# Kernel optimization log

Measured on AMD Instinct MI355X. Metric: run time of the kernel, lower is better.

Reference implementation:

```python
import jax, jax.numpy as jnp
import numpy as np

B, K, IN, CH, M, N = 1024, 64, 128, 256, 4, 16


def setup_inputs() -> dict:
    key = jax.random.key(0)
    ks = jax.random.split(key, 12)
    s = 0.02
    return {
        "user_node": jax.random.normal(ks[0], (B, K, IN), jnp.float32),
        "RIS_node": jax.random.normal(ks[1], (B, IN), jnp.float32),
        "cas_channel": jax.random.normal(ks[2], (B, K, 2 * M * N), jnp.float32),
        "d_link": jax.random.normal(ks[3], (B, K, 2 * M), jnp.float32),
        # f2_user: Linear(3*IN -> CH), ReLU, Linear(CH -> CH)
        "W1": jax.random.normal(ks[4], (3 * IN, CH), jnp.float32) * s,
        "b1": jnp.zeros((CH,), jnp.float32),
        "W2": jax.random.normal(ks[5], (CH, CH), jnp.float32) * s,
        "b2": jnp.zeros((CH,), jnp.float32),
        # f3_RIS: Linear(2*IN -> CH), ReLU, Linear(CH -> CH)
        "W3": jax.random.normal(ks[6], (2 * IN, CH), jnp.float32) * s,
        "b3": jnp.zeros((CH,), jnp.float32),
        "W4": jax.random.normal(ks[7], (CH, CH), jnp.float32) * s,
        "b4": jnp.zeros((CH,), jnp.float32),
    }


def _leave_one_out_max(x):
    # x: (B, K, D). Exact leave-one-out max via prefix/suffix cummax, O(K).
    prefix = jax.lax.cummax(x, axis=1)                      # max over 0..k
    suffix = jax.lax.cummax(x[:, ::-1], axis=1)[:, ::-1]    # max over k..K-1
    neg = jnp.full_like(x[:, :1], -jnp.inf)
    left = jnp.concatenate([neg, prefix[:, :-1]], axis=1)   # max over 0..k-1
    right = jnp.concatenate([suffix[:, 1:], neg], axis=1)   # max over k+1..K-1
    return jnp.maximum(left, right)


def reference(user_node, RIS_node, cas_channel, d_link,
              W1, b1, W2, b2, W3, b3, W4, b4):
    b, k, d = user_node.shape
    mean_user = jnp.mean(user_node, axis=1)                 # (B, IN)
    loo_max = _leave_one_out_max(user_node)                 # (B, K, IN)
    ris_b = jnp.broadcast_to(RIS_node[:, None, :], (b, k, d))
    feat = jnp.concatenate([user_node, loo_max, ris_b], axis=-1)  # (B, K, 3*IN)
    h_user = jax.nn.relu(feat @ W1 + b1) @ W2 + b2          # (B, K, CH)
    user_node_update = jnp.concatenate([user_node, h_user], axis=-1)  # (B,K,IN+CH)
    rfeat = jnp.concatenate([RIS_node, mean_user], axis=-1)  # (B, 2*IN)
    h_ris = jax.nn.relu(rfeat @ W3 + b3) @ W4 + b4          # (B, CH)
    RIS_node_update = jnp.concatenate([RIS_node, h_ris], axis=-1)    # (B, IN+CH)
    return user_node_update, RIS_node_update
```

## Files before the change

### kernel.cpp

```cpp
#include <hip/hip_runtime.h>

typedef __attribute__((ext_vector_type(8))) short short8;
typedef __attribute__((ext_vector_type(4))) float f32x4;
typedef __attribute__((ext_vector_type(4))) int i32x4;
typedef __attribute__((ext_vector_type(4))) unsigned u32x4;

__device__ __forceinline__ unsigned short f2bf(float f) {
  unsigned u = __builtin_bit_cast(unsigned, f);
  u += 0x7fffu + ((u >> 16) & 1u);
  return (unsigned short)(u >> 16);
}

__global__ __launch_bounds__(256) void prep(
    const float* __restrict__ user,
    const float* __restrict__ W1, const float* __restrict__ W2,
    const float* __restrict__ W3, const float* __restrict__ W4,
    float* __restrict__ mean, float* __restrict__ max1,
    float* __restrict__ max2, int* __restrict__ argm,
    unsigned short* __restrict__ W1f, unsigned short* __restrict__ W2f,
    unsigned short* __restrict__ W3f, unsigned short* __restrict__ W4f) {
  if (blockIdx.x < 512) {
    int idx = blockIdx.x * 256 + threadIdx.x;
    int b = idx >> 7, i = idx & 127;
    const float* up = user + (size_t)(b * 64) * 128 + i;
    float s = 0.f, m1 = -3.402823466e38f, m2 = -3.402823466e38f;
    int am = 0;
    #pragma unroll 8
    for (int k = 0; k < 64; ++k) {
      float u = up[(size_t)k * 128];
      s += u;
      if (u > m1) { m2 = m1; m1 = u; am = k; }
      else if (u > m2) { m2 = u; }
    }
    mean[idx] = s * (1.f / 64.f);
    max1[idx] = m1;
    max2[idx] = m2;
    argm[idx] = am;
  } else {
    int idx = (blockIdx.x - 512) * 256 + threadIdx.x;
    const float* src; unsigned short* dst; int kb; int rel;
    if (idx < 98304)        { src = W1; dst = W1f; kb = 12; rel = idx; }
    else if (idx < 163840)  { src = W2; dst = W2f; kb = 8;  rel = idx - 98304; }
    else if (idx < 229376)  { src = W3; dst = W3f; kb = 8;  rel = idx - 163840; }
    else                    { src = W4; dst = W4f; kb = 8;  rel = idx - 229376; }
    int kk = rel >> 8, n = rel & 255;
    int lane = (n & 15) | (((kk >> 3) & 3) << 4);
    int di = (((n >> 4) * kb + (kk >> 5)) * 64 + lane) * 8 + (kk & 7);
    dst[di] = f2bf(src[rel]);
  }
}

template<int MODE>
__device__ __forceinline__ void mlp_body(
    int bx, unsigned short* __restrict__ Abuf, unsigned short* __restrict__ Hb,
    const float* __restrict__ srcA,
    const float* __restrict__ max1, const float* __restrict__ max2,
    const int* __restrict__ argm, const float* __restrict__ aux,
    const unsigned short* __restrict__ Wa, const unsigned short* __restrict__ Wb,
    const float* __restrict__ ba, const float* __restrict__ bb,
    float* __restrict__ out) {
  constexpr int NSTEP = (MODE == 0) ? 6 : 4;
  constexpr int KB1 = NSTEP * 2;

  const int tid = threadIdx.x;
  const int lane = tid & 63, wn = tid >> 6;
  const int row0 = bx * 64;
  const int sr = tid >> 2;
  const int sc = (tid & 3) << 4;
  const int bidx = row0 >> 6;

  auto load_step = [&](int s, float* v) {
    if constexpr (MODE == 0) {
      if (s < 2) {
        const float* p = &srcA[(size_t)(row0 + sr) * 128 + s * 64 + sc];
        #pragma unroll
        for (int q = 0; q < 4; ++q) {
          f32x4 t = *(const f32x4*)(p + q * 4);
          #pragma unroll
          for (int jj = 0; jj < 4; ++jj) v[q * 4 + jj] = t[jj];
        }
      } else if (s < 4) {
        int ib = bidx * 128 + (s - 2) * 64 + sc;
        #pragma unroll
        for (int q = 0; q < 4; ++q) {
          i32x4 aq = *(const i32x4*)(argm + ib + q * 4);
          f32x4 m1q = *(const f32x4*)(max1 + ib + q * 4);
          f32x4 m2q = *(const f32x4*)(max2 + ib + q * 4);
          #pragma unroll
          for (int jj = 0; jj < 4; ++jj)
            v[q * 4 + jj] = (aq[jj] == sr) ? m2q[jj] : m1q[jj];
        }
      } else {
        const float* p = &aux[bidx * 128 + (s - 4) * 64 + sc];
        #pragma unroll
        for (int q = 0; q < 4; ++q) {
          f32x4 t = *(const f32x4*)(p + q * 4);
          #pragma unroll
          for (int jj = 0; jj < 4; ++jj) v[q * 4 + jj] = t[jj];
        }
      }
    } else {
      const float* p = (s < 2) ? &srcA[(size_t)(row0 + sr) * 128 + s * 64 + sc]
                               : &aux[(size_t)(row0 + sr) * 128 + (s - 2) * 64 + sc];
      #pragma unroll
      for (int q = 0; q < 4; ++q) {
        f32x4 t = *(const f32x4*)(p + q * 4);
        #pragma unroll
        for (int jj = 0; jj < 4; ++jj) v[q * 4 + jj] = t[jj];
      }
    }
  };

  auto stage_write = [&](int buf, int s, const float* v) {
    if (s < 2) {
      float* o = &out[(size_t)(row0 + sr) * 384 + s * 64 + sc];
      #pragma unroll
      for (int q = 0; q < 4; ++q) {
        f32x4 t = {v[q * 4 + 0], v[q * 4 + 1], v[q * 4 + 2], v[q * 4 + 3]};
        *(f32x4*)(o + q * 4) = t;
      }
    }
    unsigned pk[8];
    #pragma unroll
    for (int j = 0; j < 8; ++j)
      pk[j] = (unsigned)f2bf(v[2 * j]) | ((unsigned)f2bf(v[2 * j + 1]) << 16);
    unsigned short* base = Abuf + buf * (64 * 64) + sr * 64;
    int c0 = (tid & 3) * 2, k = sr & 7;
    u32x4 w0 = {pk[0], pk[1], pk[2], pk[3]};
    u32x4 w1 = {pk[4], pk[5], pk[6], pk[7]};
    *(u32x4*)(base + ((c0 ^ k) << 3)) = w0;
    *(u32x4*)(base + (((c0 + 1) ^ k) << 3)) = w1;
  };

  f32x4 acc[4][4];
  #pragma unroll
  for (int a = 0; a < 4; ++a)
    #pragma unroll
    for (int q = 0; q < 4; ++q) acc[a][q] = (f32x4)0.f;

  {
    float v0[16];
    load_step(0, v0);
    stage_write(0, 0, v0);
  }
  __syncthreads();
  #pragma unroll
  for (int s = 0; s < NSTEP; ++s) {
    float nv[16];
    if (s + 1 < NSTEP) load_step(s + 1, nv);
    const unsigned short* Ab = Abuf + (s & 1) * (64 * 64);
    #pragma unroll
    for (int ks = 0; ks < 2; ++ks) {
      short8 af[4], bfr[4];
      #pragma unroll
      for (int mf = 0; mf < 4; ++mf) {
        int r = mf * 16 + (lane & 15);
        int c = ks * 4 + (lane >> 4);
        af[mf] = *(const short8*)(Ab + r * 64 + ((c ^ (r & 7)) << 3));
      }
      #pragma unroll
      for (int nf = 0; nf < 4; ++nf)
        bfr[nf] = *(const short8*)&Wa[(size_t)(((wn * 4 + nf) * KB1 + (s * 2 + ks)) * 64 + lane) * 8];
      #pragma unroll
      for (int mf = 0; mf < 4; ++mf)
        #pragma unroll
        for (int nf = 0; nf < 4; ++nf)
          acc[mf][nf] = __builtin_amdgcn_mfma_f32_16x16x32_bf16(af[mf], bfr[nf], acc[mf][nf], 0, 0, 0);
    }
    if (s + 1 < NSTEP) stage_write((s + 1) & 1, s + 1, nv);
    __syncthreads();
  }

  float bav[4];
  #pragma unroll
  for (int nf = 0; nf < 4; ++nf) bav[nf] = ba[wn * 64 + nf * 16 + (lane & 15)];
  #pragma unroll
  for (int mf = 0; mf < 4; ++mf)
    #pragma unroll
    for (int nf = 0; nf < 4; ++nf)
      #pragma unroll
      for (int j = 0; j < 4; ++j) {
        int r = mf * 16 + ((lane >> 4) * 4) + j;
        int col = wn * 64 + nf * 16 + (lane & 15);
        int c = col >> 3;
        Hb[r * 256 + ((c ^ (r & 7)) << 3) + (col & 7)] =
            f2bf(fmaxf(acc[mf][nf][j] + bav[nf], 0.f));
      }
  __syncthreads();

  #pragma unroll
  for (int a = 0; a < 4; ++a)
    #pragma unroll
    for (int q = 0; q < 4; ++q) acc[a][q] = (f32x4)0.f;
  #pragma unroll
  for (int kc = 0; kc < 8; ++kc) {
    short8 af[4], bfr[4];
    #pragma unroll
    for (int mf = 0; mf < 4; ++mf) {
      int r = mf * 16 + (lane & 15);
      int c = kc * 4 + (lane >> 4);
      af[mf] = *(const short8*)(Hb + r * 256 + ((c ^ (r & 7)) << 3));
    }
    #pragma unroll
    for (int nf = 0; nf < 4; ++nf)
      bfr[nf] = *(const short8*)&Wb[(size_t)(((wn * 4 + nf) * 8 + kc) * 64 + lane) * 8];
    #pragma unroll
    for (int mf = 0; mf < 4; ++mf)
      #pragma unroll
      for (int nf = 0; nf < 4; ++nf)
        acc[mf][nf] = __builtin_amdgcn_mfma_f32_16x16x32_bf16(af[mf], bfr[nf], acc[mf][nf], 0, 0, 0);
  }

  float bbv[4];
  #pragma unroll
  for (int nf = 0; nf < 4; ++nf) bbv[nf] = bb[wn * 64 + nf * 16 + (lane & 15)];
  #pragma unroll
  for (int mf = 0; mf < 4; ++mf)
    #pragma unroll
    for (int nf = 0; nf < 4; ++nf)
      #pragma unroll
      for (int j = 0; j < 4; ++j) {
        int r = mf * 16 + ((lane >> 4) * 4) + j;
        int col = wn * 64 + nf * 16 + (lane & 15);
        out[(size_t)(row0 + r) * 384 + 128 + col] = acc[mf][nf][j] + bbv[nf];
      }
}

__global__ __launch_bounds__(256, 3) void fused(
    const float* __restrict__ user, const float* __restrict__ ris,
    const float* __restrict__ max1, const float* __restrict__ max2,
    const int* __restrict__ argm, const float* __restrict__ mean,
    const unsigned short* __restrict__ W1f, const unsigned short* __restrict__ W2f,
    const unsigned short* __restrict__ W3f, const unsigned short* __restrict__ W4f,
    const float* __restrict__ b1, const float* __restrict__ b2,
    const float* __restrict__ b3, const float* __restrict__ b4,
    float* __restrict__ out0, float* __restrict__ out1) {
  __shared__ unsigned short Abuf[2 * 64 * 64];
  __shared__ unsigned short Hb[64 * 256];
  if (blockIdx.x < 1024)
    mlp_body<0>(blockIdx.x, Abuf, Hb, user, max1, max2, argm, ris,
                W1f, W2f, b1, b2, out0);
  else
    mlp_body<1>(blockIdx.x - 1024, Abuf, Hb, ris, nullptr, nullptr, nullptr,
                mean, W3f, W4f, b3, b4, out1);
}

extern "C" void kernel_launch(void* const* d_in, const int* in_sizes, int n_in,
                              void* d_out, int out_size, void* d_ws, size_t ws_size,
                              hipStream_t stream) {
  const float* user = (const float*)d_in[0];
  const float* ris  = (const float*)d_in[1];
  const float* W1 = (const float*)d_in[4];
  const float* b1 = (const float*)d_in[5];
  const float* W2 = (const float*)d_in[6];
  const float* b2 = (const float*)d_in[7];
  const float* W3 = (const float*)d_in[8];
  const float* b3 = (const float*)d_in[9];
  const float* W4 = (const float*)d_in[10];
  const float* b4 = (const float*)d_in[11];

  float* out0 = (float*)d_out;
  float* out1 = out0 + (size_t)65536 * 384;

  char* ws = (char*)d_ws;
  float* mean = (float*)(ws);
  float* max1 = (float*)(ws + 524288);
  float* max2 = (float*)(ws + 1048576);
  int*   argm = (int*)(ws + 1572864);
  unsigned short* W1f = (unsigned short*)(ws + 2097152);
  unsigned short* W2f = (unsigned short*)(ws + 2293760);
  unsigned short* W3f = (unsigned short*)(ws + 2424832);
  unsigned short* W4f = (unsigned short*)(ws + 2555904);

  hipLaunchKernelGGL(prep, dim3(1664), dim3(256), 0, stream,
                     user, W1, W2, W3, W4, mean, max1, max2, argm,
                     W1f, W2f, W3f, W4f);
  hipLaunchKernelGGL(fused, dim3(1040), dim3(256), 0, stream,
                     user, ris, max1, max2, argm, mean,
                     W1f, W2f, W3f, W4f, b1, b2, b3, b4, out0, out1);
}
```

Baseline: 71.90 us.

## Load GEMM1 A-fragments directly from global, drop LDS staging, precompute bf16 stats

The first GEMM no longer stages its A operand through double-buffered shared memory. Each lane loads its MFMA fragment straight from global memory (user rows converted to bf16 on the fly, and the max, mean and ris vectors stored as bf16 by prep), which removes the per-step __syncthreads. The passthrough copies of user and ris into the outputs move into the prep kernel, and occupancy is raised to 4 blocks per SM because less LDS is needed. In exchange, global loads are less coalesced and sit on the MFMA critical path with no software prefetch.

```diff
diff --git a/kernel.cpp b/kernel.cpp
--- a/kernel.cpp
+++ b/kernel.cpp
@@ -3,7 +3,6 @@
 typedef __attribute__((ext_vector_type(8))) short short8;
 typedef __attribute__((ext_vector_type(4))) float f32x4;
 typedef __attribute__((ext_vector_type(4))) int i32x4;
-typedef __attribute__((ext_vector_type(4))) unsigned u32x4;
 
 __device__ __forceinline__ unsigned short f2bf(float f) {
   unsigned u = __builtin_bit_cast(unsigned, f);
@@ -12,30 +11,37 @@
 }
 
 __global__ __launch_bounds__(256) void prep(
-    const float* __restrict__ user,
+    const float* __restrict__ user, const float* __restrict__ ris,
     const float* __restrict__ W1, const float* __restrict__ W2,
     const float* __restrict__ W3, const float* __restrict__ W4,
-    float* __restrict__ mean, float* __restrict__ max1,
-    float* __restrict__ max2, int* __restrict__ argm,
+    unsigned short* __restrict__ m1b, unsigned short* __restrict__ m2b,
+    int* __restrict__ am, unsigned short* __restrict__ meanb,
+    unsigned short* __restrict__ risb,
     unsigned short* __restrict__ W1f, unsigned short* __restrict__ W2f,
-    unsigned short* __restrict__ W3f, unsigned short* __restrict__ W4f) {
+    unsigned short* __restrict__ W3f, unsigned short* __restrict__ W4f,
+    float* __restrict__ out0, float* __restrict__ out1) {
   if (blockIdx.x < 512) {
     int idx = blockIdx.x * 256 + threadIdx.x;
     int b = idx >> 7, i = idx & 127;
     const float* up = user + (size_t)(b * 64) * 128 + i;
+    float* op = out0 + (size_t)(b * 64) * 384 + i;
     float s = 0.f, m1 = -3.402823466e38f, m2 = -3.402823466e38f;
-    int am = 0;
+    int amx = 0;
     #pragma unroll 8
     for (int k = 0; k < 64; ++k) {
       float u = up[(size_t)k * 128];
+      op[(size_t)k * 384] = u;
       s += u;
-      if (u > m1) { m2 = m1; m1 = u; am = k; }
+      if (u > m1) { m2 = m1; m1 = u; amx = k; }
       else if (u > m2) { m2 = u; }
     }
-    mean[idx] = s * (1.f / 64.f);
-    max1[idx] = m1;
-    max2[idx] = m2;
-    argm[idx] = am;
+    m1b[idx] = f2bf(m1);
+    m2b[idx] = f2bf(m2);
+    am[idx] = amx;
+    meanb[idx] = f2bf(s * (1.f / 64.f));
+    float rv = ris[idx];
+    out1[(size_t)b * 384 + i] = rv;
+    risb[idx] = f2bf(rv);
   } else {
     int idx = (blockIdx.x - 512) * 256 + threadIdx.x;
     const float* src; unsigned short* dst; int kb; int rel;
@@ -52,124 +58,81 @@
 
 template<int MODE>
 __device__ __forceinline__ void mlp_body(
-    int bx, unsigned short* __restrict__ Abuf, unsigned short* __restrict__ Hb,
-    const float* __restrict__ srcA,
-    const float* __restrict__ max1, const float* __restrict__ max2,
-    const int* __restrict__ argm, const float* __restrict__ aux,
+    int bx, unsigned short* __restrict__ Hb,
+    const float* __restrict__ user,
+    const unsigned short* __restrict__ m1b, const unsigned short* __restrict__ m2b,
+    const int* __restrict__ am,
+    const unsigned short* __restrict__ risb, const unsigned short* __restrict__ meanb,
     const unsigned short* __restrict__ Wa, const unsigned short* __restrict__ Wb,
     const float* __restrict__ ba, const float* __restrict__ bb,
     float* __restrict__ out) {
-  constexpr int NSTEP = (MODE == 0) ? 6 : 4;
-  constexpr int KB1 = NSTEP * 2;
+  constexpr int NFS = (MODE == 0) ? 12 : 8;
 
   const int tid = threadIdx.x;
   const int lane = tid & 63, wn = tid >> 6;
   const int row0 = bx * 64;
-  const int sr = tid >> 2;
-  const int sc = (tid & 3) << 4;
-  const int bidx = row0 >> 6;
-
-  auto load_step = [&](int s, float* v) {
+  const int r = lane & 15;
+  const int k8 = (lane >> 4) * 8;
+
+  f32x4 acc[4][4];
+  #pragma unroll
+  for (int a = 0; a < 4; ++a)
+    #pragma unroll
+    for (int q = 0; q < 4; ++q) acc[a][q] = (f32x4)0.f;
+
+  #pragma unroll
+  for (int fs = 0; fs < NFS; ++fs) {
+    short8 af[4];
     if constexpr (MODE == 0) {
-      if (s < 2) {
-        const float* p = &srcA[(size_t)(row0 + sr) * 128 + s * 64 + sc];
+      if (fs < 4) {
         #pragma unroll
-        for (int q = 0; q < 4; ++q) {
-          f32x4 t = *(const f32x4*)(p + q * 4);
+        for (int mf = 0; mf < 4; ++mf) {
+          const float* p = &user[(size_t)(row0 + mf * 16 + r) * 128 + fs * 32 + k8];
+          f32x4 t0 = *(const f32x4*)p;
+          f32x4 t1 = *(const f32x4*)(p + 4);
+          short8 t;
           #pragma unroll
-          for (int jj = 0; jj < 4; ++jj) v[q * 4 + jj] = t[jj];
+          for (int j = 0; j < 4; ++j) { t[j] = (short)f2bf(t0[j]); t[4 + j] = (short)f2bf(t1[j]); }
+          af[mf] = t;
         }
-      } else if (s < 4) {
-        int ib = bidx * 128 + (s - 2) * 64 + sc;
+      } else if (fs < 8) {
+        int c0 = bx * 128 + (fs - 4) * 32 + k8;
+        short8 m1v = *(const short8*)&m1b[c0];
+        short8 m2v = *(const short8*)&m2b[c0];
+        i32x4 a0 = *(const i32x4*)&am[c0];
+        i32x4 a1 = *(const i32x4*)&am[c0 + 4];
         #pragma unroll
-        for (int q = 0; q < 4; ++q) {
-          i32x4 aq = *(const i32x4*)(argm + ib + q * 4);
-          f32x4 m1q = *(const f32x4*)(max1 + ib + q * 4);
-          f32x4 m2q = *(const f32x4*)(max2 + ib + q * 4);
+        for (int mf = 0; mf < 4; ++mf) {
+          int rr = mf * 16 + r;
+          short8 t;
           #pragma unroll
-          for (int jj = 0; jj < 4; ++jj)
-            v[q * 4 + jj] = (aq[jj] == sr) ? m2q[jj] : m1q[jj];
+          for (int j = 0; j < 4; ++j) {
+            t[j]     = (a0[j] == rr) ? m2v[j]     : m1v[j];
+            t[4 + j] = (a1[j] == rr) ? m2v[4 + j] : m1v[4 + j];
+          }
+          af[mf] = t;
         }
       } else {
-        const float* p = &aux[bidx * 128 + (s - 4) * 64 + sc];
+        short8 v = *(const short8*)&risb[bx * 128 + (fs - 8) * 32 + k8];
         #pragma unroll
-        for (int q = 0; q < 4; ++q) {
-          f32x4 t = *(const f32x4*)(p + q * 4);
-          #pragma unroll
-          for (int jj = 0; jj < 4; ++jj) v[q * 4 + jj] = t[jj];
-        }
+        for (int mf = 0; mf < 4; ++mf) af[mf] = v;
       }
     } else {
-      const float* p = (s < 2) ? &srcA[(size_t)(row0 + sr) * 128 + s * 64 + sc]
-                               : &aux[(size_t)(row0 + sr) * 128 + (s - 2) * 64 + sc];
-      #pragma unroll
-      for (int q = 0; q < 4; ++q) {
-        f32x4 t = *(const f32x4*)(p + q * 4);
-        #pragma unroll
-        for (int jj = 0; jj < 4; ++jj) v[q * 4 + jj] = t[jj];
-      }
+      const unsigned short* src = (fs < 4) ? risb : meanb;
+      #pragma unroll
+      for (int mf = 0; mf < 4; ++mf)
+        af[mf] = *(const short8*)&src[(size_t)(row0 + mf * 16 + r) * 128 + (fs & 3) * 32 + k8];
     }
-  };
-
-  auto stage_write = [&](int buf, int s, const float* v) {
-    if (s < 2) {
-      float* o = &out[(size_t)(row0 + sr) * 384 + s * 64 + sc];
-      #pragma unroll
-      for (int q = 0; q < 4; ++q) {
-        f32x4 t = {v[q * 4 + 0], v[q * 4 + 1], v[q * 4 + 2], v[q * 4 + 3]};
-        *(f32x4*)(o + q * 4) = t;
-      }
-    }
-    unsigned pk[8];
-    #pragma unroll
-    for (int j = 0; j < 8; ++j)
-      pk[j] = (unsigned)f2bf(v[2 * j]) | ((unsigned)f2bf(v[2 * j + 1]) << 16);
-    unsigned short* base = Abuf + buf * (64 * 64) + sr * 64;
-    int c0 = (tid & 3) * 2, k = sr & 7;
-    u32x4 w0 = {pk[0], pk[1], pk[2], pk[3]};
-    u32x4 w1 = {pk[4], pk[5], pk[6], pk[7]};
-    *(u32x4*)(base + ((c0 ^ k) << 3)) = w0;
-    *(u32x4*)(base + (((c0 + 1) ^ k) << 3)) = w1;
-  };
-
-  f32x4 acc[4][4];
-  #pragma unroll
-  for (int a = 0; a < 4; ++a)
-    #pragma unroll
-    for (int q = 0; q < 4; ++q) acc[a][q] = (f32x4)0.f;
-
-  {
-    float v0[16];
-    load_step(0, v0);
-    stage_write(0, 0, v0);
+    short8 bfr[4];
+    #pragma unroll
+    for (int nf = 0; nf < 4; ++nf)
+      bfr[nf] = *(const short8*)&Wa[(size_t)(((wn * 4 + nf) * NFS + fs) * 64 + lane) * 8];
+    #pragma unroll
+    for (int mf = 0; mf < 4; ++mf)
+      #pragma unroll
+      for (int nf = 0; nf < 4; ++nf)
+        acc[mf][nf] = __builtin_amdgcn_mfma_f32_16x16x32_bf16(af[mf], bfr[nf], acc[mf][nf], 0, 0, 0);
   }
-  __syncthreads();
-  #pragma unroll
-  for (int s = 0; s < NSTEP; ++s) {
-    float nv[16];
-    if (s + 1 < NSTEP) load_step(s + 1, nv);
-    const unsigned short* Ab = Abuf + (s & 1) * (64 * 64);
-    #pragma unroll
-    for (int ks = 0; ks < 2; ++ks) {
-      short8 af[4], bfr[4];
-      #pragma unroll
-      for (int mf = 0; mf < 4; ++mf) {
-        int r = mf * 16 + (lane & 15);
-        int c = ks * 4 + (lane >> 4);
-        af[mf] = *(const short8*)(Ab + r * 64 + ((c ^ (r & 7)) << 3));
-      }
-      #pragma unroll
-      for (int nf = 0; nf < 4; ++nf)
-        bfr[nf] = *(const short8*)&Wa[(size_t)(((wn * 4 + nf) * KB1 + (s * 2 + ks)) * 64 + lane) * 8];
-      #pragma unroll
-      for (int mf = 0; mf < 4; ++mf)
-        #pragma unroll
-        for (int nf = 0; nf < 4; ++nf)
-          acc[mf][nf] = __builtin_amdgcn_mfma_f32_16x16x32_bf16(af[mf], bfr[nf], acc[mf][nf], 0, 0, 0);
-    }
-    if (s + 1 < NSTEP) stage_write((s + 1) & 1, s + 1, nv);
-    __syncthreads();
-  }
 
   float bav[4];
   #pragma unroll
@@ -180,10 +143,10 @@
     for (int nf = 0; nf < 4; ++nf)
       #pragma unroll
       for (int j = 0; j < 4; ++j) {
-        int r = mf * 16 + ((lane >> 4) * 4) + j;
+        int rr = mf * 16 + ((lane >> 4) * 4) + j;
         int col = wn * 64 + nf * 16 + (lane & 15);
         int c = col >> 3;
-        Hb[r * 256 + ((c ^ (r & 7)) << 3) + (col & 7)] =
+        Hb[rr * 256 + ((c ^ (rr & 7)) << 3) + (col & 7)] =
             f2bf(fmaxf(acc[mf][nf][j] + bav[nf], 0.f));
       }
   __syncthreads();
@@ -197,9 +160,9 @@
     short8 af[4], bfr[4];
     #pragma unroll
     for (int mf = 0; mf < 4; ++mf) {
-      int r = mf * 16 + (lane & 15);
+      int rr = mf * 16 + (lane & 15);
       int c = kc * 4 + (lane >> 4);
-      af[mf] = *(const short8*)(Hb + r * 256 + ((c ^ (r & 7)) << 3));
+      af[mf] = *(const short8*)(Hb + rr * 256 + ((c ^ (rr & 7)) << 3));
     }
     #pragma unroll
     for (int nf = 0; nf < 4; ++nf)
@@ -220,29 +183,29 @@
     for (int nf = 0; nf < 4; ++nf)
       #pragma unroll
       for (int j = 0; j < 4; ++j) {
-        int r = mf * 16 + ((lane >> 4) * 4) + j;
+        int rr = mf * 16 + ((lane >> 4) * 4) + j;
         int col = wn * 64 + nf * 16 + (lane & 15);
-        out[(size_t)(row0 + r) * 384 + 128 + col] = acc[mf][nf][j] + bbv[nf];
+        out[(size_t)(row0 + rr) * 384 + 128 + col] = acc[mf][nf][j] + bbv[nf];
       }
 }
 
-__global__ __launch_bounds__(256, 3) void fused(
-    const float* __restrict__ user, const float* __restrict__ ris,
-    const float* __restrict__ max1, const float* __restrict__ max2,
-    const int* __restrict__ argm, const float* __restrict__ mean,
+__global__ __launch_bounds__(256, 4) void fused(
+    const float* __restrict__ user,
+    const unsigned short* __restrict__ m1b, const unsigned short* __restrict__ m2b,
+    const int* __restrict__ am,
+    const unsigned short* __restrict__ risb, const unsigned short* __restrict__ meanb,
     const unsigned short* __restrict__ W1f, const unsigned short* __restrict__ W2f,
     const unsigned short* __restrict__ W3f, const unsigned short* __restrict__ W4f,
     const float* __restrict__ b1, const float* __restrict__ b2,
     const float* __restrict__ b3, const float* __restrict__ b4,
     float* __restrict__ out0, float* __restrict__ out1) {
-  __shared__ unsigned short Abuf[2 * 64 * 64];
   __shared__ unsigned short Hb[64 * 256];
   if (blockIdx.x < 1024)
-    mlp_body<0>(blockIdx.x, Abuf, Hb, user, max1, max2, argm, ris,
+    mlp_body<0>(blockIdx.x, Hb, user, m1b, m2b, am, risb, meanb,
                 W1f, W2f, b1, b2, out0);
   else
-    mlp_body<1>(blockIdx.x - 1024, Abuf, Hb, ris, nullptr, nullptr, nullptr,
-                mean, W3f, W4f, b3, b4, out1);
+    mlp_body<1>(blockIdx.x - 1024, Hb, user, m1b, m2b, am, risb, meanb,
+                W3f, W4f, b3, b4, out1);
 }
 
 extern "C" void kernel_launch(void* const* d_in, const int* in_sizes, int n_in,
@@ -263,19 +226,21 @@
   float* out1 = out0 + (size_t)65536 * 384;
 
   char* ws = (char*)d_ws;
-  float* mean = (float*)(ws);
-  float* max1 = (float*)(ws + 524288);
-  float* max2 = (float*)(ws + 1048576);
-  int*   argm = (int*)(ws + 1572864);
-  unsigned short* W1f = (unsigned short*)(ws + 2097152);
-  unsigned short* W2f = (unsigned short*)(ws + 2293760);
-  unsigned short* W3f = (unsigned short*)(ws + 2424832);
-  unsigned short* W4f = (unsigned short*)(ws + 2555904);
+  unsigned short* m1b   = (unsigned short*)(ws);
+  unsigned short* m2b   = (unsigned short*)(ws + 262144);
+  int*            amv   = (int*)(ws + 524288);
+  unsigned short* meanb = (unsigned short*)(ws + 1048576);
+  unsigned short* risb  = (unsigned short*)(ws + 1310720);
+  unsigned short* W1f   = (unsigned short*)(ws + 1572864);
+  unsigned short* W2f   = (unsigned short*)(ws + 1769472);
+  unsigned short* W3f   = (unsigned short*)(ws + 1900544);
+  unsigned short* W4f   = (unsigned short*)(ws + 2031616);
 
   hipLaunchKernelGGL(prep, dim3(1664), dim3(256), 0, stream,
-                     user, W1, W2, W3, W4, mean, max1, max2, argm,
-                     W1f, W2f, W3f, W4f);
+                     user, ris, W1, W2, W3, W4,
+                     m1b, m2b, amv, meanb, risb,
+                     W1f, W2f, W3f, W4f, out0, out1);
   hipLaunchKernelGGL(fused, dim3(1040), dim3(256), 0, stream,
-                     user, ris, max1, max2, argm, mean,
+                     user, m1b, m2b, amv, risb, meanb,
                      W1f, W2f, W3f, W4f, b1, b2, b3, b4, out0, out1);
 }
```

Result: slower. 80.67 us (+12.2%).
